# Performance work log

Measured on AMD Instinct MI355X. Metric: run time of the kernel, lower is better.

Reference implementation:

```python
import jax, jax.numpy as jnp
import numpy as np


def setup_inputs() -> dict:
    key = jax.random.key(0)
    ks = jax.random.split(key, 6)
    B, T, D, H = 64, 2048, 128, 256
    stdv = 1.0 / np.sqrt(H)
    return {
        "X": jax.random.normal(ks[0], (B, T, D), dtype=jnp.float32),
        "W": jax.random.normal(ks[1], (D, 4 * H), dtype=jnp.float32) * stdv,
        "U": jax.random.normal(ks[2], (H, 4 * H), dtype=jnp.float32) * stdv,
        "bias": jax.random.normal(ks[3], (4 * H,), dtype=jnp.float32) * stdv,
        "h0": jax.random.normal(ks[4], (B, H), dtype=jnp.float32) * stdv,
        "c0": jax.random.normal(ks[5], (B, H), dtype=jnp.float32) * stdv,
    }


def reference(X, W, U, bias, h0, c0):
    HS = U.shape[0]
    # Hoist input projection into one big GEMM: [B,T,4H]
    xW = jnp.einsum("btd,dg->btg", X, W) + bias

    def step(carry, xw_t):
        h, c = carry
        gates = xw_t + h @ U  # [B,4H]
        i_t = jax.nn.sigmoid(gates[:, :HS])
        f_t = jax.nn.sigmoid(gates[:, HS:2 * HS])
        g_t = jnp.tanh(gates[:, 2 * HS:3 * HS])
        o_t = jax.nn.sigmoid(gates[:, 3 * HS:])
        c_new = f_t * c + i_t * g_t
        h_new = o_t * jnp.tanh(c_new)
        return (h_new, c_new), h_new

    (h_t, c_t), hs = jax.lax.scan(step, (h0, c0), jnp.swapaxes(xW, 0, 1))
    hidden_seq = jnp.swapaxes(hs, 0, 1)  # [B,T,H]
    return (hidden_seq, (h_t, c_t))
```

## Files before the change

### kernel.cpp

```cpp
#include <hip/hip_runtime.h>
#include <hip/hip_bf16.h>

#define BB 64
#define TT 2048
#define DD 128
#define HH 256
#define G4 1024
#define TC 16

typedef _Float16 half2_t __attribute__((ext_vector_type(2)));

#if __has_builtin(__builtin_amdgcn_fdot2)
#define FDOT2(a, b, c) __builtin_amdgcn_fdot2((a), (b), (c), false)
#else
__device__ __forceinline__ float FDOT2(half2_t a, half2_t b, float c) {
    return c + (float)a[0] * (float)b[0] + (float)a[1] * (float)b[1];
}
#endif

__device__ __forceinline__ half2_t u2h(unsigned int u) {
    union { unsigned int u; half2_t h; } x; x.u = u; return x.h;
}
__device__ __forceinline__ unsigned int pkf16(float a, float b) {
    union { _Float16 h[2]; unsigned int u; } x;
    x.h[0] = (_Float16)a; x.h[1] = (_Float16)b; return x.u;
}
__device__ __forceinline__ unsigned short f16b(float a) {
    union { _Float16 h; unsigned short u; } x; x.h = (_Float16)a; return x.u;
}
__device__ __forceinline__ float sigf(float x) {
    return 1.0f / (1.0f + __expf(-x));
}
__device__ __forceinline__ float tanh_fast(float x) {
    return 1.0f - 2.0f / (__expf(2.0f * x) + 1.0f);
}
__device__ __forceinline__ void bar_lgkm() {
    asm volatile("s_waitcnt lgkmcnt(0)\n\ts_barrier" ::: "memory");
}

__global__ void zero_hglob(unsigned long long* hglob) {
    hglob[blockIdx.x * 256 + threadIdx.x] = 0ull;
}

__global__ void __launch_bounds__(128)
pack_slices(const float* __restrict__ src, unsigned short* __restrict__ dst, int K)
{
    const int g = blockIdx.x, kb = blockIdx.y, c = threadIdx.x;
    const int gc = ((c >> 5) << 8) + (g << 5) + (c & 31);
    unsigned int* d32 = (unsigned int*)dst;
    const int dbase = ((g << 7) + c) * K + kb * 64;
    for (int kk = 0; kk < 64; kk += 2) {
        const float a = src[(size_t)(kb * 64 + kk) * G4 + gc];
        const float b = src[(size_t)(kb * 64 + kk + 1) * G4 + gc];
        d32[(dbase + kk) >> 1] = pkf16(a, b);
    }
}

extern "C" __global__ void __launch_bounds__(512, 2)
lstm_fuse(const float* __restrict__ X, const unsigned short* __restrict__ Upack,
          const unsigned short* __restrict__ Wpack, const float* __restrict__ bias,
          const float* __restrict__ h0, const float* __restrict__ c0,
          unsigned long long* __restrict__ hglob, float* __restrict__ out)
{
    __shared__ __align__(16) uint4 Ulds4[128 * 32];
    __shared__ __align__(16) uint4 Wlds4[128 * 16];
    __shared__ float xw[2][TC][128];
    __shared__ __align__(16) unsigned short Xs[2 * TC * DD];
    __shared__ float gvp[2][4][128];
    __shared__ __align__(16) unsigned short hsh[2 * HH];

    const int pair = blockIdx.x & 31;
    const int g = blockIdx.x >> 5;
    const int b0 = pair * 2;
    const int tid = threadIdx.x;
    const int wave = tid >> 6, lane = tid & 63;
    const int c = tid & 127, s = tid >> 7;

    {
        const uint4* Usrc = (const uint4*)(Upack + (size_t)g * 32768);
        #pragma unroll
        for (int i = 0; i < 8; ++i) {
            const int idx = i * 512 + tid;
            const int cc = idx >> 5, gr = idx & 31;
            Ulds4[cc * 32 + (gr ^ (cc & 31))] = Usrc[idx];
        }
        const uint4* Wsrc = (const uint4*)(Wpack + (size_t)g * 16384);
        #pragma unroll
        for (int i = 0; i < 4; ++i) {
            const int idx = i * 512 + tid;
            const int cc = idx >> 4, gr = idx & 15;
            Wlds4[cc * 16 + (gr ^ (cc & 15))] = Wsrc[idx];
        }
    }
    hsh[tid] = f16b(h0[(size_t)(b0 + (tid >> 8)) * HH + (tid & 255)]);
    float c_reg = 0.0f, h_last = 0.0f;
    if (wave == 0) {
        const int p = lane >> 5, j = lane & 31;
        c_reg = c0[(size_t)(b0 + p) * HH + (g << 5) + j];
        h_last = h0[(size_t)(b0 + p) * HH + (g << 5) + j];
    }
    const float bc = bias[((c >> 5) << 8) + (g << 5) + (c & 31)];
    __syncthreads();

    const size_t obase0 = (size_t)b0 * TT * HH + (g << 5);
    const size_t obase1 = (size_t)(b0 + 1) * TT * HH + (g << 5);
    const int slotbase = ((pair << 3) + g) << 1;

    for (int chunk = 0; chunk < TT / TC; ++chunk) {
        const int t0 = chunk * TC;

        #pragma unroll
        for (int r = 0; r < 2; ++r) {
            const float4 xv = ((const float4*)(X + ((size_t)(b0 + r) * TT + t0) * DD))[tid];
            ((uint2*)Xs)[r * 512 + tid] = make_uint2(pkf16(xv.x, xv.y), pkf16(xv.z, xv.w));
        }
        bar_lgkm();

        {
            const int p = s >> 1, th = s & 1;
            float acc[8];
            #pragma unroll
            for (int t = 0; t < 8; ++t) acc[t] = bc;
            #pragma unroll
            for (int k8 = 0; k8 < 16; ++k8) {
                const uint4 w4 = Wlds4[c * 16 + (k8 ^ (c & 15))];
                #pragma unroll
                for (int t = 0; t < 8; ++t) {
                    const uint4 xg = *(const uint4*)((const char*)Xs +
                                     ((p * 16 + th * 8 + t) << 8) + (k8 << 4));
                    acc[t] = FDOT2(u2h(xg.x), u2h(w4.x), acc[t]);
                    acc[t] = FDOT2(u2h(xg.y), u2h(w4.y), acc[t]);
                    acc[t] = FDOT2(u2h(xg.z), u2h(w4.z), acc[t]);
                    acc[t] = FDOT2(u2h(xg.w), u2h(w4.w), acc[t]);
                }
            }
            #pragma unroll
            for (int t = 0; t < 8; ++t) xw[p][th * 8 + t][c] = acc[t];
        }
        bar_lgkm();

        for (int tt2 = 0; tt2 < TC; ++tt2) {
            const int tau = t0 + tt2;

            {
                float a0 = (s == 0) ? xw[0][tt2][c] : 0.0f;
                float a1 = (s == 0) ? xw[1][tt2][c] : 0.0f;
                #pragma unroll
                for (int ii = 0; ii < 8; ++ii) {
                    const uint4 ug = Ulds4[c * 32 + ((s * 8 + ii) ^ (c & 31))];
                    const uint4 hg0 = *(const uint4*)((const char*)hsh + (s << 7) + (ii << 4));
                    const uint4 hg1 = *(const uint4*)((const char*)hsh + 512 + (s << 7) + (ii << 4));
                    a0 = FDOT2(u2h(ug.x), u2h(hg0.x), a0);
                    a1 = FDOT2(u2h(ug.x), u2h(hg1.x), a1);
                    a0 = FDOT2(u2h(ug.y), u2h(hg0.y), a0);
                    a1 = FDOT2(u2h(ug.y), u2h(hg1.y), a1);
                    a0 = FDOT2(u2h(ug.z), u2h(hg0.z), a0);
                    a1 = FDOT2(u2h(ug.z), u2h(hg1.z), a1);
                    a0 = FDOT2(u2h(ug.w), u2h(hg0.w), a0);
                    a1 = FDOT2(u2h(ug.w), u2h(hg1.w), a1);
                }
                gvp[0][s][c] = a0;
                gvp[1][s][c] = a1;
            }
            bar_lgkm();

            const int par = (tau + 1) & 1;
            if (wave == 0) {
                const int p = lane >> 5, j = lane & 31;
                const float* gv = &gvp[p][0][0];
                float gi = 0.f, gf = 0.f, gg = 0.f, go = 0.f;
                #pragma unroll
                for (int q = 0; q < 4; ++q) {
                    gi += gv[q * 128 + j];       gf += gv[q * 128 + 32 + j];
                    gg += gv[q * 128 + 64 + j];  go += gv[q * 128 + 96 + j];
                }
                const float it = sigf(gi), ft = sigf(gf);
                const float gt = tanh_fast(gg), ot = sigf(go);
                c_reg = fmaf(ft, c_reg, it * gt);
                const float hn = ot * tanh_fast(c_reg);
                h_last = hn;
                const unsigned int hu = f16b(hn);
                const unsigned int lo = __shfl((int)hu, j);
                const unsigned int hi = __shfl((int)hu, j + 32);
                if (lane < 32) {
                    const unsigned long long pkt =
                        ((unsigned long long)(unsigned)(tau + 1) << 32) |
                        ((unsigned long long)hi << 16) | (unsigned long long)lo;
                    __hip_atomic_store(&hglob[(size_t)(slotbase + par) * 32 + j],
                                       pkt, __ATOMIC_RELAXED, __HIP_MEMORY_SCOPE_AGENT);
                }
                out[(p ? obase1 : obase0) + (size_t)tau * HH + j] = hn;
                hsh[(p << 8) + (g << 5) + j] = (unsigned short)hu;
            } else if (tau < TT - 1 && lane < 32) {
                const int pg = (g + wave) & 7;
                const unsigned long long* q =
                    &hglob[(size_t)((((pair << 3) + pg) << 1) + par) * 32 + lane];
                __builtin_amdgcn_s_sleep(2);
                unsigned long long v; int spins = 0;
                do {
                    v = __hip_atomic_load(q, __ATOMIC_RELAXED, __HIP_MEMORY_SCOPE_AGENT);
                    if (++spins > (1 << 20)) break;
                } while ((unsigned)(v >> 32) != (unsigned)(tau + 1));
                hsh[(pg << 5) + lane] = (unsigned short)(v & 0xffff);
                hsh[256 + (pg << 5) + lane] = (unsigned short)((v >> 16) & 0xffff);
            }
            bar_lgkm();
        }
    }

    if (wave == 0) {
        const int p = lane >> 5, j = lane & 31;
        const size_t base = (size_t)BB * TT * HH;
        out[base + (size_t)(b0 + p) * HH + (g << 5) + j] = h_last;
        out[base + (size_t)BB * HH + (size_t)(b0 + p) * HH + (g << 5) + j] = c_reg;
    }
}

extern "C" __global__ void __launch_bounds__(512)
lstm_persist(const float* __restrict__ X, const float* __restrict__ W,
             const float* __restrict__ U, const float* __restrict__ bias,
             const float* __restrict__ h0, const float* __restrict__ c0,
             float* __restrict__ out)
{
    __shared__ float xw[TC][G4];
    __shared__ float Xs[TC][DD];
    __shared__ float hsh[HH];
    __shared__ float gv[G4];

    const int b = blockIdx.x;
    const int tid = threadIdx.x;
    const float2* __restrict__ U2 = reinterpret_cast<const float2*>(U);
    const float2* __restrict__ W2 = reinterpret_cast<const float2*>(W);

    float c_reg = 0.0f;
    if (tid < HH) { hsh[tid] = h0[b * HH + tid]; c_reg = c0[b * HH + tid]; }
    const float2 bs = reinterpret_cast<const float2*>(bias)[tid];
    __syncthreads();

    for (int chunk = 0; chunk < TT / TC; ++chunk) {
        const int t0 = chunk * TC;
        {
            const float4* src = reinterpret_cast<const float4*>(X + ((size_t)b * TT + t0) * DD);
            float4* dst = reinterpret_cast<float4*>(&Xs[0][0]);
            for (int i = tid; i < TC * DD / 4; i += 512) dst[i] = src[i];
        }
        __syncthreads();
        float acc0[TC], acc1[TC];
        #pragma unroll
        for (int t = 0; t < TC; ++t) { acc0[t] = bs.x; acc1[t] = bs.y; }
        for (int kk = 0; kk < DD; kk += 4) {
            const float2 w0 = W2[(size_t)(kk + 0) * (G4 / 2) + tid];
            const float2 w1 = W2[(size_t)(kk + 1) * (G4 / 2) + tid];
            const float2 w2 = W2[(size_t)(kk + 2) * (G4 / 2) + tid];
            const float2 w3 = W2[(size_t)(kk + 3) * (G4 / 2) + tid];
            #pragma unroll
            for (int t = 0; t < TC; ++t) {
                const float4 xv = *reinterpret_cast<const float4*>(&Xs[t][kk]);
                acc0[t] = fmaf(xv.x, w0.x, acc0[t]); acc1[t] = fmaf(xv.x, w0.y, acc1[t]);
                acc0[t] = fmaf(xv.y, w1.x, acc0[t]); acc1[t] = fmaf(xv.y, w1.y, acc1[t]);
                acc0[t] = fmaf(xv.z, w2.x, acc0[t]); acc1[t] = fmaf(xv.z, w2.y, acc1[t]);
                acc0[t] = fmaf(xv.w, w3.x, acc0[t]); acc1[t] = fmaf(xv.w, w3.y, acc1[t]);
            }
        }
        #pragma unroll
        for (int t = 0; t < TC; ++t)
            *reinterpret_cast<float2*>(&xw[t][2 * tid]) = make_float2(acc0[t], acc1[t]);
        __syncthreads();

        for (int t = 0; t < TC; ++t) {
            const float2 x2 = *reinterpret_cast<const float2*>(&xw[t][2 * tid]);
            float a0 = x2.x, a1 = x2.y;
            #pragma unroll 4
            for (int k = 0; k < HH; k += 4) {
                const float4 hk = *reinterpret_cast<const float4*>(&hsh[k]);
                const float2 u0 = U2[(size_t)(k + 0) * (G4 / 2) + tid];
                const float2 u1 = U2[(size_t)(k + 1) * (G4 / 2) + tid];
                const float2 u2 = U2[(size_t)(k + 2) * (G4 / 2) + tid];
                const float2 u3 = U2[(size_t)(k + 3) * (G4 / 2) + tid];
                a0 = fmaf(hk.x, u0.x, a0); a1 = fmaf(hk.x, u0.y, a1);
                a0 = fmaf(hk.y, u1.x, a0); a1 = fmaf(hk.y, u1.y, a1);
                a0 = fmaf(hk.z, u2.x, a0); a1 = fmaf(hk.z, u2.y, a1);
                a0 = fmaf(hk.w, u3.x, a0); a1 = fmaf(hk.w, u3.y, a1);
            }
            *reinterpret_cast<float2*>(&gv[2 * tid]) = make_float2(a0, a1);
            __syncthreads();
            if (tid < HH) {
                const float it = sigf(gv[tid]);
                const float ft = sigf(gv[tid + HH]);
                const float gt = tanh_fast(gv[tid + 2 * HH]);
                const float ot = sigf(gv[tid + 3 * HH]);
                c_reg = fmaf(ft, c_reg, it * gt);
                const float hn = ot * tanh_fast(c_reg);
                hsh[tid] = hn;
                out[((size_t)b * TT + (t0 + t)) * HH + tid] = hn;
            }
            __syncthreads();
        }
    }
    if (tid < HH) {
        const size_t base = (size_t)BB * TT * HH;
        out[base + (size_t)b * HH + tid] = hsh[tid];
        out[base + (size_t)BB * HH + (size_t)b * HH + tid] = c_reg;
    }
}

extern "C" void kernel_launch(void* const* d_in, const int* in_sizes, int n_in,
                              void* d_out, int out_size, void* d_ws, size_t ws_size,
                              hipStream_t stream) {
    const float* X    = (const float*)d_in[0];
    const float* W    = (const float*)d_in[1];
    const float* U    = (const float*)d_in[2];
    const float* bias = (const float*)d_in[3];
    const float* h0   = (const float*)d_in[4];
    const float* c0   = (const float*)d_in[5];
    float* out = (float*)d_out;
    (void)in_sizes; (void)n_in; (void)out_size;

    const size_t upk = 512 * 1024;
    const size_t wpk = 256 * 1024;
    const size_t mbx = 128 * 1024;

    if (ws_size >= upk + wpk + mbx) {
        unsigned short* Upack = (unsigned short*)d_ws;
        unsigned short* Wpack = (unsigned short*)((char*)d_ws + upk);
        unsigned long long* hglob = (unsigned long long*)((char*)d_ws + upk + wpk);
        zero_hglob<<<dim3(64), dim3(256), 0, stream>>>(hglob);
        pack_slices<<<dim3(8, 4), dim3(128), 0, stream>>>(U, Upack, 256);
        pack_slices<<<dim3(8, 2), dim3(128), 0, stream>>>(W, Wpack, 128);
        lstm_fuse<<<dim3(256), dim3(512), 0, stream>>>(
            X, Upack, Wpack, bias, h0, c0, hglob, out);
        return;
    }

    lstm_persist<<<dim3(BB), dim3(512), 0, stream>>>(X, W, U, bias, h0, c0, out);
}
```

Baseline: 3.568 ms.

## Widen LSTM recurrent blocks to 1024 threads with eight-way K split

Doubles the threads per block from 512 to 1024. The recurrent h@U dot product is now split over 8 K-slices instead of 4, and the input projection over 4 timestep groups per batch row. The xW term moves from the first partial sum into the gate reduction in wave 0. Peer-h polling now uses two redundant trains of 7 waves, one with a longer sleep, to cut the latency of seeing a neighbour's update. This shortens the per-step serial dot-product chain, at the cost of more partial-sum reduction, more LDS traffic, and one block per CU under the new launch bounds.

```diff
diff --git a/kernel.cpp b/kernel.cpp
--- a/kernel.cpp
+++ b/kernel.cpp
@@ -56,8 +56,8 @@
     }
 }
 
-extern "C" __global__ void __launch_bounds__(512, 2)
-lstm_fuse(const float* __restrict__ X, const unsigned short* __restrict__ Upack,
+extern "C" __global__ void __launch_bounds__(1024, 1)
+lstm_wide(const float* __restrict__ X, const unsigned short* __restrict__ Upack,
           const unsigned short* __restrict__ Wpack, const float* __restrict__ bias,
           const float* __restrict__ h0, const float* __restrict__ c0,
           unsigned long long* __restrict__ hglob, float* __restrict__ out)
@@ -66,7 +66,7 @@
     __shared__ __align__(16) uint4 Wlds4[128 * 16];
     __shared__ float xw[2][TC][128];
     __shared__ __align__(16) unsigned short Xs[2 * TC * DD];
-    __shared__ float gvp[2][4][128];
+    __shared__ float gvp[2][8][128];
     __shared__ __align__(16) unsigned short hsh[2 * HH];
 
     const int pair = blockIdx.x & 31;
@@ -79,20 +79,21 @@
     {
         const uint4* Usrc = (const uint4*)(Upack + (size_t)g * 32768);
         #pragma unroll
-        for (int i = 0; i < 8; ++i) {
-            const int idx = i * 512 + tid;
+        for (int i = 0; i < 4; ++i) {
+            const int idx = i * 1024 + tid;
             const int cc = idx >> 5, gr = idx & 31;
             Ulds4[cc * 32 + (gr ^ (cc & 31))] = Usrc[idx];
         }
         const uint4* Wsrc = (const uint4*)(Wpack + (size_t)g * 16384);
         #pragma unroll
-        for (int i = 0; i < 4; ++i) {
-            const int idx = i * 512 + tid;
+        for (int i = 0; i < 2; ++i) {
+            const int idx = i * 1024 + tid;
             const int cc = idx >> 4, gr = idx & 15;
             Wlds4[cc * 16 + (gr ^ (cc & 15))] = Wsrc[idx];
         }
     }
-    hsh[tid] = f16b(h0[(size_t)(b0 + (tid >> 8)) * HH + (tid & 255)]);
+    if (tid < 512)
+        hsh[tid] = f16b(h0[(size_t)(b0 + (tid >> 8)) * HH + (tid & 255)]);
     float c_reg = 0.0f, h_last = 0.0f;
     if (wave == 0) {
         const int p = lane >> 5, j = lane & 31;
@@ -111,23 +112,23 @@
 
         #pragma unroll
         for (int r = 0; r < 2; ++r) {
-            const float4 xv = ((const float4*)(X + ((size_t)(b0 + r) * TT + t0) * DD))[tid];
-            ((uint2*)Xs)[r * 512 + tid] = make_uint2(pkf16(xv.x, xv.y), pkf16(xv.z, xv.w));
+            const float2 v = ((const float2*)(X + ((size_t)(b0 + r) * TT + t0) * DD))[tid];
+            ((unsigned int*)Xs)[r * 1024 + tid] = pkf16(v.x, v.y);
         }
         bar_lgkm();
 
         {
-            const int p = s >> 1, th = s & 1;
-            float acc[8];
+            const int p = s >> 2, tq = s & 3;
+            float acc[4];
             #pragma unroll
-            for (int t = 0; t < 8; ++t) acc[t] = bc;
+            for (int t = 0; t < 4; ++t) acc[t] = bc;
             #pragma unroll
             for (int k8 = 0; k8 < 16; ++k8) {
                 const uint4 w4 = Wlds4[c * 16 + (k8 ^ (c & 15))];
                 #pragma unroll
-                for (int t = 0; t < 8; ++t) {
+                for (int t = 0; t < 4; ++t) {
                     const uint4 xg = *(const uint4*)((const char*)Xs +
-                                     ((p * 16 + th * 8 + t) << 8) + (k8 << 4));
+                                     ((p * 16 + tq * 4 + t) << 8) + (k8 << 4));
                     acc[t] = FDOT2(u2h(xg.x), u2h(w4.x), acc[t]);
                     acc[t] = FDOT2(u2h(xg.y), u2h(w4.y), acc[t]);
                     acc[t] = FDOT2(u2h(xg.z), u2h(w4.z), acc[t]);
@@ -135,7 +136,7 @@
                 }
             }
             #pragma unroll
-            for (int t = 0; t < 8; ++t) xw[p][th * 8 + t][c] = acc[t];
+            for (int t = 0; t < 4; ++t) xw[p][tq * 4 + t][c] = acc[t];
         }
         bar_lgkm();
 
@@ -143,13 +144,13 @@
             const int tau = t0 + tt2;
 
             {
-                float a0 = (s == 0) ? xw[0][tt2][c] : 0.0f;
-                float a1 = (s == 0) ? xw[1][tt2][c] : 0.0f;
+                float a0 = 0.0f, a1 = 0.0f;
                 #pragma unroll
-                for (int ii = 0; ii < 8; ++ii) {
-                    const uint4 ug = Ulds4[c * 32 + ((s * 8 + ii) ^ (c & 31))];
-                    const uint4 hg0 = *(const uint4*)((const char*)hsh + (s << 7) + (ii << 4));
-                    const uint4 hg1 = *(const uint4*)((const char*)hsh + 512 + (s << 7) + (ii << 4));
+                for (int ii = 0; ii < 4; ++ii) {
+                    const int k8 = s * 4 + ii;
+                    const uint4 ug = Ulds4[c * 32 + (k8 ^ (c & 31))];
+                    const uint4 hg0 = *(const uint4*)((const char*)hsh + (k8 << 4));
+                    const uint4 hg1 = *(const uint4*)((const char*)hsh + 512 + (k8 << 4));
                     a0 = FDOT2(u2h(ug.x), u2h(hg0.x), a0);
                     a1 = FDOT2(u2h(ug.x), u2h(hg1.x), a1);
                     a0 = FDOT2(u2h(ug.y), u2h(hg0.y), a0);
@@ -167,12 +168,14 @@
             const int par = (tau + 1) & 1;
             if (wave == 0) {
                 const int p = lane >> 5, j = lane & 31;
-                const float* gv = &gvp[p][0][0];
-                float gi = 0.f, gf = 0.f, gg = 0.f, go = 0.f;
+                float gi = xw[p][tt2][j];
+                float gf = xw[p][tt2][32 + j];
+                float gg = xw[p][tt2][64 + j];
+                float go = xw[p][tt2][96 + j];
                 #pragma unroll
-                for (int q = 0; q < 4; ++q) {
-                    gi += gv[q * 128 + j];       gf += gv[q * 128 + 32 + j];
-                    gg += gv[q * 128 + 64 + j];  go += gv[q * 128 + 96 + j];
+                for (int q = 0; q < 8; ++q) {
+                    gi += gvp[p][q][j];       gf += gvp[p][q][32 + j];
+                    gg += gvp[p][q][64 + j];  go += gvp[p][q][96 + j];
                 }
                 const float it = sigf(gi), ft = sigf(gf);
                 const float gt = tanh_fast(gg), ot = sigf(go);
@@ -191,11 +194,13 @@
                 }
                 out[(p ? obase1 : obase0) + (size_t)tau * HH + j] = hn;
                 hsh[(p << 8) + (g << 5) + j] = (unsigned short)hu;
-            } else if (tau < TT - 1 && lane < 32) {
-                const int pg = (g + wave) & 7;
+            } else if (wave <= 14 && tau < TT - 1 && lane < 32) {
+                const int pw = ((wave - 1) % 7) + 1;
+                const int train = (wave - 1) / 7;
+                const int pg = (g + pw) & 7;
                 const unsigned long long* q =
                     &hglob[(size_t)((((pair << 3) + pg) << 1) + par) * 32 + lane];
-                __builtin_amdgcn_s_sleep(2);
+                if (train) __builtin_amdgcn_s_sleep(6);
                 unsigned long long v; int spins = 0;
                 do {
                     v = __hip_atomic_load(q, __ATOMIC_RELAXED, __HIP_MEMORY_SCOPE_AGENT);
@@ -327,7 +332,7 @@
         zero_hglob<<<dim3(64), dim3(256), 0, stream>>>(hglob);
         pack_slices<<<dim3(8, 4), dim3(128), 0, stream>>>(U, Upack, 256);
         pack_slices<<<dim3(8, 2), dim3(128), 0, stream>>>(W, Wpack, 128);
-        lstm_fuse<<<dim3(256), dim3(512), 0, stream>>>(
+        lstm_wide<<<dim3(256), dim3(1024), 0, stream>>>(
             X, Upack, Wpack, bias, h0, c0, hglob, out);
         return;
     }
```

New measurement: 4.074 ms. 1.14x slower.

## Distribute recurrent matvec per source wave to cut per-step barriers

Applied to the files above, without the earlier changes.

Each wave now computes the partial h·U contribution for the 32-column h slice it owns: wave 0 handles its own freshly computed slice, and the other waves handle the neighbour slices they poll from global memory. Partial sums are written into double-buffered gvp[nxt] and reduced in the next step together with xw. This removes one block barrier per timestep and overlaps the matvec with the cross-block exchange. The cost is a larger reduction (8 partials) and more LDS traffic per step, and launch bounds drop to one block per CU.

```diff
diff --git a/kernel.cpp b/kernel.cpp
--- a/kernel.cpp
+++ b/kernel.cpp
@@ -36,6 +36,9 @@
 }
 __device__ __forceinline__ void bar_lgkm() {
     asm volatile("s_waitcnt lgkmcnt(0)\n\ts_barrier" ::: "memory");
+}
+__device__ __forceinline__ void wait_lgkm() {
+    asm volatile("s_waitcnt lgkmcnt(0)" ::: "memory");
 }
 
 __global__ void zero_hglob(unsigned long long* hglob) {
@@ -56,8 +59,8 @@
     }
 }
 
-extern "C" __global__ void __launch_bounds__(512, 2)
-lstm_fuse(const float* __restrict__ X, const unsigned short* __restrict__ Upack,
+extern "C" __global__ void __launch_bounds__(512, 1)
+lstm_dist(const float* __restrict__ X, const unsigned short* __restrict__ Upack,
           const unsigned short* __restrict__ Wpack, const float* __restrict__ bias,
           const float* __restrict__ h0, const float* __restrict__ c0,
           unsigned long long* __restrict__ hglob, float* __restrict__ out)
@@ -66,8 +69,9 @@
     __shared__ __align__(16) uint4 Wlds4[128 * 16];
     __shared__ float xw[2][TC][128];
     __shared__ __align__(16) unsigned short Xs[2 * TC * DD];
-    __shared__ float gvp[2][4][128];
-    __shared__ __align__(16) unsigned short hsh[2 * HH];
+    __shared__ float gvp[2][2][8][128];
+    __shared__ __align__(16) unsigned short hst0[8][32];
+    __shared__ __align__(16) unsigned short hst1[8][32];
 
     const int pair = blockIdx.x & 31;
     const int g = blockIdx.x >> 5;
@@ -92,7 +96,6 @@
             Wlds4[cc * 16 + (gr ^ (cc & 15))] = Wsrc[idx];
         }
     }
-    hsh[tid] = f16b(h0[(size_t)(b0 + (tid >> 8)) * HH + (tid & 255)]);
     float c_reg = 0.0f, h_last = 0.0f;
     if (wave == 0) {
         const int p = lane >> 5, j = lane & 31;
@@ -100,6 +103,35 @@
         h_last = h0[(size_t)(b0 + p) * HH + (g << 5) + j];
     }
     const float bc = bias[((c >> 5) << 8) + (g << 5) + (c & 31)];
+
+    {
+        const int pg = (g + wave) & 7;
+        if (lane < 32) {
+            hst0[wave][lane] = f16b(h0[(size_t)b0 * HH + (pg << 5) + lane]);
+            hst1[wave][lane] = f16b(h0[(size_t)(b0 + 1) * HH + (pg << 5) + lane]);
+        }
+        wait_lgkm();
+        const int c0l = lane, c1l = lane + 64;
+        float a00 = 0.f, a01 = 0.f, a10 = 0.f, a11 = 0.f;
+        #pragma unroll
+        for (int ks = 0; ks < 4; ++ks) {
+            const int k8 = (pg << 2) + ks;
+            const uint4 u0 = Ulds4[c0l * 32 + (k8 ^ (c0l & 31))];
+            const uint4 u1 = Ulds4[c1l * 32 + (k8 ^ (c1l & 31))];
+            const uint4 hv0 = *(const uint4*)((const char*)&hst0[wave][0] + (ks << 4));
+            const uint4 hv1 = *(const uint4*)((const char*)&hst1[wave][0] + (ks << 4));
+            a00 = FDOT2(u2h(u0.x), u2h(hv0.x), a00); a01 = FDOT2(u2h(u0.x), u2h(hv1.x), a01);
+            a10 = FDOT2(u2h(u1.x), u2h(hv0.x), a10); a11 = FDOT2(u2h(u1.x), u2h(hv1.x), a11);
+            a00 = FDOT2(u2h(u0.y), u2h(hv0.y), a00); a01 = FDOT2(u2h(u0.y), u2h(hv1.y), a01);
+            a10 = FDOT2(u2h(u1.y), u2h(hv0.y), a10); a11 = FDOT2(u2h(u1.y), u2h(hv1.y), a11);
+            a00 = FDOT2(u2h(u0.z), u2h(hv0.z), a00); a01 = FDOT2(u2h(u0.z), u2h(hv1.z), a01);
+            a10 = FDOT2(u2h(u1.z), u2h(hv0.z), a10); a11 = FDOT2(u2h(u1.z), u2h(hv1.z), a11);
+            a00 = FDOT2(u2h(u0.w), u2h(hv0.w), a00); a01 = FDOT2(u2h(u0.w), u2h(hv1.w), a01);
+            a10 = FDOT2(u2h(u1.w), u2h(hv0.w), a10); a11 = FDOT2(u2h(u1.w), u2h(hv1.w), a11);
+        }
+        gvp[0][0][wave][c0l] = a00;  gvp[0][1][wave][c0l] = a01;
+        gvp[0][0][wave][c1l] = a10;  gvp[0][1][wave][c1l] = a11;
+    }
     __syncthreads();
 
     const size_t obase0 = (size_t)b0 * TT * HH + (g << 5);
@@ -140,69 +172,94 @@
         bar_lgkm();
 
         for (int tt2 = 0; tt2 < TC; ++tt2) {
-            const int tau = t0 + tt2;
-
-            {
-                float a0 = (s == 0) ? xw[0][tt2][c] : 0.0f;
-                float a1 = (s == 0) ? xw[1][tt2][c] : 0.0f;
-                #pragma unroll
-                for (int ii = 0; ii < 8; ++ii) {
-                    const uint4 ug = Ulds4[c * 32 + ((s * 8 + ii) ^ (c & 31))];
-                    const uint4 hg0 = *(const uint4*)((const char*)hsh + (s << 7) + (ii << 4));
-                    const uint4 hg1 = *(const uint4*)((const char*)hsh + 512 + (s << 7) + (ii << 4));
-                    a0 = FDOT2(u2h(ug.x), u2h(hg0.x), a0);
-                    a1 = FDOT2(u2h(ug.x), u2h(hg1.x), a1);
-                    a0 = FDOT2(u2h(ug.y), u2h(hg0.y), a0);
-                    a1 = FDOT2(u2h(ug.y), u2h(hg1.y), a1);
-                    a0 = FDOT2(u2h(ug.z), u2h(hg0.z), a0);
-                    a1 = FDOT2(u2h(ug.z), u2h(hg1.z), a1);
-                    a0 = FDOT2(u2h(ug.w), u2h(hg0.w), a0);
-                    a1 = FDOT2(u2h(ug.w), u2h(hg1.w), a1);
-                }
-                gvp[0][s][c] = a0;
-                gvp[1][s][c] = a1;
-            }
-            bar_lgkm();
-
-            const int par = (tau + 1) & 1;
+            const int it = t0 + tt2;
+            const int cur = it & 1, nxt = cur ^ 1;
+            const int par = (it + 1) & 1;
+
             if (wave == 0) {
                 const int p = lane >> 5, j = lane & 31;
-                const float* gv = &gvp[p][0][0];
-                float gi = 0.f, gf = 0.f, gg = 0.f, go = 0.f;
+                const float* xr = &xw[p][tt2][0];
+                float gi = xr[j], gf = xr[32 + j], gg = xr[64 + j], go = xr[96 + j];
                 #pragma unroll
-                for (int q = 0; q < 4; ++q) {
-                    gi += gv[q * 128 + j];       gf += gv[q * 128 + 32 + j];
-                    gg += gv[q * 128 + 64 + j];  go += gv[q * 128 + 96 + j];
-                }
-                const float it = sigf(gi), ft = sigf(gf);
+                for (int q = 0; q < 8; ++q) {
+                    const float* gq = &gvp[cur][p][q][0];
+                    gi += gq[j]; gf += gq[32 + j]; gg += gq[64 + j]; go += gq[96 + j];
+                }
+                const float it_g = sigf(gi), ft = sigf(gf);
                 const float gt = tanh_fast(gg), ot = sigf(go);
-                c_reg = fmaf(ft, c_reg, it * gt);
+                c_reg = fmaf(ft, c_reg, it_g * gt);
                 const float hn = ot * tanh_fast(c_reg);
                 h_last = hn;
                 const unsigned int hu = f16b(hn);
                 const unsigned int lo = __shfl((int)hu, j);
                 const unsigned int hi = __shfl((int)hu, j + 32);
-                if (lane < 32) {
+                if (it < TT - 1 && lane < 32) {
                     const unsigned long long pkt =
-                        ((unsigned long long)(unsigned)(tau + 1) << 32) |
+                        ((unsigned long long)(unsigned)(it + 1) << 32) |
                         ((unsigned long long)hi << 16) | (unsigned long long)lo;
                     __hip_atomic_store(&hglob[(size_t)(slotbase + par) * 32 + j],
                                        pkt, __ATOMIC_RELAXED, __HIP_MEMORY_SCOPE_AGENT);
-                }
-                out[(p ? obase1 : obase0) + (size_t)tau * HH + j] = hn;
-                hsh[(p << 8) + (g << 5) + j] = (unsigned short)hu;
-            } else if (tau < TT - 1 && lane < 32) {
+                    hst0[0][j] = (unsigned short)lo;
+                    hst1[0][j] = (unsigned short)hi;
+                }
+                out[(p ? obase1 : obase0) + (size_t)it * HH + j] = hn;
+                if (it < TT - 1) {
+                    wait_lgkm();
+                    const int c0l = lane, c1l = lane + 64;
+                    float a00 = 0.f, a01 = 0.f, a10 = 0.f, a11 = 0.f;
+                    #pragma unroll
+                    for (int ks = 0; ks < 4; ++ks) {
+                        const int k8 = (g << 2) + ks;
+                        const uint4 u0 = Ulds4[c0l * 32 + (k8 ^ (c0l & 31))];
+                        const uint4 u1 = Ulds4[c1l * 32 + (k8 ^ (c1l & 31))];
+                        const uint4 hv0 = *(const uint4*)((const char*)&hst0[0][0] + (ks << 4));
+                        const uint4 hv1 = *(const uint4*)((const char*)&hst1[0][0] + (ks << 4));
+                        a00 = FDOT2(u2h(u0.x), u2h(hv0.x), a00); a01 = FDOT2(u2h(u0.x), u2h(hv1.x), a01);
+                        a10 = FDOT2(u2h(u1.x), u2h(hv0.x), a10); a11 = FDOT2(u2h(u1.x), u2h(hv1.x), a11);
+                        a00 = FDOT2(u2h(u0.y), u2h(hv0.y), a00); a01 = FDOT2(u2h(u0.y), u2h(hv1.y), a01);
+                        a10 = FDOT2(u2h(u1.y), u2h(hv0.y), a10); a11 = FDOT2(u2h(u1.y), u2h(hv1.y), a11);
+                        a00 = FDOT2(u2h(u0.z), u2h(hv0.z), a00); a01 = FDOT2(u2h(u0.z), u2h(hv1.z), a01);
+                        a10 = FDOT2(u2h(u1.z), u2h(hv0.z), a10); a11 = FDOT2(u2h(u1.z), u2h(hv1.z), a11);
+                        a00 = FDOT2(u2h(u0.w), u2h(hv0.w), a00); a01 = FDOT2(u2h(u0.w), u2h(hv1.w), a01);
+                        a10 = FDOT2(u2h(u1.w), u2h(hv0.w), a10); a11 = FDOT2(u2h(u1.w), u2h(hv1.w), a11);
+                    }
+                    gvp[nxt][0][0][c0l] = a00;  gvp[nxt][1][0][c0l] = a01;
+                    gvp[nxt][0][0][c1l] = a10;  gvp[nxt][1][0][c1l] = a11;
+                }
+            } else if (it < TT - 1) {
                 const int pg = (g + wave) & 7;
-                const unsigned long long* q =
-                    &hglob[(size_t)((((pair << 3) + pg) << 1) + par) * 32 + lane];
-                __builtin_amdgcn_s_sleep(2);
-                unsigned long long v; int spins = 0;
-                do {
-                    v = __hip_atomic_load(q, __ATOMIC_RELAXED, __HIP_MEMORY_SCOPE_AGENT);
-                    if (++spins > (1 << 20)) break;
-                } while ((unsigned)(v >> 32) != (unsigned)(tau + 1));
-                hsh[(pg << 5) + lane] = (unsigned short)(v & 0xffff);
-                hsh[256 + (pg << 5) + lane] = (unsigned short)((v >> 16) & 0xffff);
+                if (lane < 32) {
+                    const unsigned long long* q =
+                        &hglob[(size_t)((((pair << 3) + pg) << 1) + par) * 32 + lane];
+                    unsigned long long v; int spins = 0;
+                    do {
+                        v = __hip_atomic_load(q, __ATOMIC_RELAXED, __HIP_MEMORY_SCOPE_AGENT);
+                        if (++spins > (1 << 20)) break;
+                    } while ((unsigned)(v >> 32) != (unsigned)(it + 1));
+                    hst0[wave][lane] = (unsigned short)(v & 0xffff);
+                    hst1[wave][lane] = (unsigned short)((v >> 16) & 0xffff);
+                }
+                wait_lgkm();
+                const int c0l = lane, c1l = lane + 64;
+                float a00 = 0.f, a01 = 0.f, a10 = 0.f, a11 = 0.f;
+                #pragma unroll
+                for (int ks = 0; ks < 4; ++ks) {
+                    const int k8 = (pg << 2) + ks;
+                    const uint4 u0 = Ulds4[c0l * 32 + (k8 ^ (c0l & 31))];
+                    const uint4 u1 = Ulds4[c1l * 32 + (k8 ^ (c1l & 31))];
+                    const uint4 hv0 = *(const uint4*)((const char*)&hst0[wave][0] + (ks << 4));
+                    const uint4 hv1 = *(const uint4*)((const char*)&hst1[wave][0] + (ks << 4));
+                    a00 = FDOT2(u2h(u0.x), u2h(hv0.x), a00); a01 = FDOT2(u2h(u0.x), u2h(hv1.x), a01);
+                    a10 = FDOT2(u2h(u1.x), u2h(hv0.x), a10); a11 = FDOT2(u2h(u1.x), u2h(hv1.x), a11);
+                    a00 = FDOT2(u2h(u0.y), u2h(hv0.y), a00); a01 = FDOT2(u2h(u0.y), u2h(hv1.y), a01);
+                    a10 = FDOT2(u2h(u1.y), u2h(hv0.y), a10); a11 = FDOT2(u2h(u1.y), u2h(hv1.y), a11);
+                    a00 = FDOT2(u2h(u0.z), u2h(hv0.z), a00); a01 = FDOT2(u2h(u0.z), u2h(hv1.z), a01);
+                    a10 = FDOT2(u2h(u1.z), u2h(hv0.z), a10); a11 = FDOT2(u2h(u1.z), u2h(hv1.z), a11);
+                    a00 = FDOT2(u2h(u0.w), u2h(hv0.w), a00); a01 = FDOT2(u2h(u0.w), u2h(hv1.w), a01);
+                    a10 = FDOT2(u2h(u1.w), u2h(hv0.w), a10); a11 = FDOT2(u2h(u1.w), u2h(hv1.w), a11);
+                }
+                gvp[nxt][0][wave][c0l] = a00;  gvp[nxt][1][wave][c0l] = a01;
+                gvp[nxt][0][wave][c1l] = a10;  gvp[nxt][1][wave][c1l] = a11;
             }
             bar_lgkm();
         }
@@ -327,7 +384,7 @@
         zero_hglob<<<dim3(64), dim3(256), 0, stream>>>(hglob);
         pack_slices<<<dim3(8, 4), dim3(128), 0, stream>>>(U, Upack, 256);
         pack_slices<<<dim3(8, 2), dim3(128), 0, stream>>>(W, Wpack, 128);
-        lstm_fuse<<<dim3(256), dim3(512), 0, stream>>>(
+        lstm_dist<<<dim3(256), dim3(512), 0, stream>>>(
             X, Upack, Wpack, bias, h0, c0, hglob, out);
         return;
     }
```

New measurement: 3.624 ms. About the same (+1.6%).

## Stagger two batch rows per block to overlap recurrence exchange with compute

Applied to the files above, without the earlier changes.

Each block now processes its two batch rows in alternating half-steps. Row 0's matvec runs while row 1's hidden-state slices from peer blocks are still arriving, and the reverse, so the cross-block spin-wait latency is hidden behind the other row's compute. Mailbox slots are split per row, each carrying an fp32 h value, which doubles the mailbox workspace and the zeroing grid. It also raises the priority of the activation wave and removes the sleep before polling. The cost is twice as many barriers per time step and narrower per-step work.

```diff
diff --git a/kernel.cpp b/kernel.cpp
--- a/kernel.cpp
+++ b/kernel.cpp
@@ -57,7 +57,7 @@
 }
 
 extern "C" __global__ void __launch_bounds__(512, 2)
-lstm_fuse(const float* __restrict__ X, const unsigned short* __restrict__ Upack,
+lstm_pipe(const float* __restrict__ X, const unsigned short* __restrict__ Upack,
           const unsigned short* __restrict__ Wpack, const float* __restrict__ bias,
           const float* __restrict__ h0, const float* __restrict__ c0,
           unsigned long long* __restrict__ hglob, float* __restrict__ out)
@@ -66,7 +66,7 @@
     __shared__ __align__(16) uint4 Wlds4[128 * 16];
     __shared__ float xw[2][TC][128];
     __shared__ __align__(16) unsigned short Xs[2 * TC * DD];
-    __shared__ float gvp[2][4][128];
+    __shared__ float gvp[4][128];
     __shared__ __align__(16) unsigned short hsh[2 * HH];
 
     const int pair = blockIdx.x & 31;
@@ -93,11 +93,12 @@
         }
     }
     hsh[tid] = f16b(h0[(size_t)(b0 + (tid >> 8)) * HH + (tid & 255)]);
-    float c_reg = 0.0f, h_last = 0.0f;
-    if (wave == 0) {
-        const int p = lane >> 5, j = lane & 31;
-        c_reg = c0[(size_t)(b0 + p) * HH + (g << 5) + j];
-        h_last = h0[(size_t)(b0 + p) * HH + (g << 5) + j];
+    float c_reg0 = 0.0f, c_reg1 = 0.0f, h_last0 = 0.0f, h_last1 = 0.0f;
+    if (wave == 0 && lane < 32) {
+        c_reg0 = c0[(size_t)b0 * HH + (g << 5) + lane];
+        c_reg1 = c0[(size_t)(b0 + 1) * HH + (g << 5) + lane];
+        h_last0 = h0[(size_t)b0 * HH + (g << 5) + lane];
+        h_last1 = h0[(size_t)(b0 + 1) * HH + (g << 5) + lane];
     }
     const float bc = bias[((c >> 5) << 8) + (g << 5) + (c & 31)];
     __syncthreads();
@@ -143,76 +144,117 @@
             const int tau = t0 + tt2;
 
             {
-                float a0 = (s == 0) ? xw[0][tt2][c] : 0.0f;
-                float a1 = (s == 0) ? xw[1][tt2][c] : 0.0f;
+                float a = (s == 0) ? xw[0][tt2][c] : 0.0f;
                 #pragma unroll
                 for (int ii = 0; ii < 8; ++ii) {
                     const uint4 ug = Ulds4[c * 32 + ((s * 8 + ii) ^ (c & 31))];
-                    const uint4 hg0 = *(const uint4*)((const char*)hsh + (s << 7) + (ii << 4));
-                    const uint4 hg1 = *(const uint4*)((const char*)hsh + 512 + (s << 7) + (ii << 4));
-                    a0 = FDOT2(u2h(ug.x), u2h(hg0.x), a0);
-                    a1 = FDOT2(u2h(ug.x), u2h(hg1.x), a1);
-                    a0 = FDOT2(u2h(ug.y), u2h(hg0.y), a0);
-                    a1 = FDOT2(u2h(ug.y), u2h(hg1.y), a1);
-                    a0 = FDOT2(u2h(ug.z), u2h(hg0.z), a0);
-                    a1 = FDOT2(u2h(ug.z), u2h(hg1.z), a1);
-                    a0 = FDOT2(u2h(ug.w), u2h(hg0.w), a0);
-                    a1 = FDOT2(u2h(ug.w), u2h(hg1.w), a1);
-                }
-                gvp[0][s][c] = a0;
-                gvp[1][s][c] = a1;
+                    const uint4 hg = *(const uint4*)((const char*)hsh + (s << 7) + (ii << 4));
+                    a = FDOT2(u2h(ug.x), u2h(hg.x), a);
+                    a = FDOT2(u2h(ug.y), u2h(hg.y), a);
+                    a = FDOT2(u2h(ug.z), u2h(hg.z), a);
+                    a = FDOT2(u2h(ug.w), u2h(hg.w), a);
+                }
+                gvp[s][c] = a;
             }
             bar_lgkm();
 
-            const int par = (tau + 1) & 1;
             if (wave == 0) {
-                const int p = lane >> 5, j = lane & 31;
-                const float* gv = &gvp[p][0][0];
-                float gi = 0.f, gf = 0.f, gg = 0.f, go = 0.f;
-                #pragma unroll
-                for (int q = 0; q < 4; ++q) {
-                    gi += gv[q * 128 + j];       gf += gv[q * 128 + 32 + j];
-                    gg += gv[q * 128 + 64 + j];  go += gv[q * 128 + 96 + j];
-                }
-                const float it = sigf(gi), ft = sigf(gf);
-                const float gt = tanh_fast(gg), ot = sigf(go);
-                c_reg = fmaf(ft, c_reg, it * gt);
-                const float hn = ot * tanh_fast(c_reg);
-                h_last = hn;
-                const unsigned int hu = f16b(hn);
-                const unsigned int lo = __shfl((int)hu, j);
-                const unsigned int hi = __shfl((int)hu, j + 32);
+                __builtin_amdgcn_s_setprio(1);
                 if (lane < 32) {
+                    const int j = lane;
+                    float gi = 0.f, gf = 0.f, gg = 0.f, go = 0.f;
+                    #pragma unroll
+                    for (int q = 0; q < 4; ++q) {
+                        gi += gvp[q][j];       gf += gvp[q][32 + j];
+                        gg += gvp[q][64 + j];  go += gvp[q][96 + j];
+                    }
+                    const float it = sigf(gi), ft = sigf(gf);
+                    const float gt = tanh_fast(gg), ot = sigf(go);
+                    c_reg0 = fmaf(ft, c_reg0, it * gt);
+                    const float hn = ot * tanh_fast(c_reg0);
+                    h_last0 = hn;
                     const unsigned long long pkt =
                         ((unsigned long long)(unsigned)(tau + 1) << 32) |
-                        ((unsigned long long)hi << 16) | (unsigned long long)lo;
-                    __hip_atomic_store(&hglob[(size_t)(slotbase + par) * 32 + j],
+                        (unsigned long long)__float_as_uint(hn);
+                    __hip_atomic_store(&hglob[(size_t)(slotbase + ((tau + 1) & 1)) * 64 + j],
                                        pkt, __ATOMIC_RELAXED, __HIP_MEMORY_SCOPE_AGENT);
-                }
-                out[(p ? obase1 : obase0) + (size_t)tau * HH + j] = hn;
-                hsh[(p << 8) + (g << 5) + j] = (unsigned short)hu;
+                    out[obase0 + (size_t)tau * HH + j] = hn;
+                    hsh[(g << 5) + j] = f16b(hn);
+                }
+                __builtin_amdgcn_s_setprio(0);
+            } else if (tau >= 1 && lane < 32) {
+                const int pg = (g + wave) & 7;
+                const unsigned long long* q =
+                    &hglob[(size_t)((((pair << 3) + pg) << 1) + (tau & 1)) * 64 + 32 + lane];
+                unsigned long long v; int spins = 0;
+                do {
+                    v = __hip_atomic_load(q, __ATOMIC_RELAXED, __HIP_MEMORY_SCOPE_AGENT);
+                    if (++spins > (1 << 20)) break;
+                } while ((unsigned)(v >> 32) != (unsigned)tau);
+                hsh[256 + (pg << 5) + lane] = f16b(__uint_as_float((unsigned)v));
+            }
+            bar_lgkm();
+
+            {
+                float a = (s == 0) ? xw[1][tt2][c] : 0.0f;
+                #pragma unroll
+                for (int ii = 0; ii < 8; ++ii) {
+                    const uint4 ug = Ulds4[c * 32 + ((s * 8 + ii) ^ (c & 31))];
+                    const uint4 hg = *(const uint4*)((const char*)hsh + 512 + (s << 7) + (ii << 4));
+                    a = FDOT2(u2h(ug.x), u2h(hg.x), a);
+                    a = FDOT2(u2h(ug.y), u2h(hg.y), a);
+                    a = FDOT2(u2h(ug.z), u2h(hg.z), a);
+                    a = FDOT2(u2h(ug.w), u2h(hg.w), a);
+                }
+                gvp[s][c] = a;
+            }
+            bar_lgkm();
+
+            if (wave == 0) {
+                __builtin_amdgcn_s_setprio(1);
+                if (lane < 32) {
+                    const int j = lane;
+                    float gi = 0.f, gf = 0.f, gg = 0.f, go = 0.f;
+                    #pragma unroll
+                    for (int q = 0; q < 4; ++q) {
+                        gi += gvp[q][j];       gf += gvp[q][32 + j];
+                        gg += gvp[q][64 + j];  go += gvp[q][96 + j];
+                    }
+                    const float it = sigf(gi), ft = sigf(gf);
+                    const float gt = tanh_fast(gg), ot = sigf(go);
+                    c_reg1 = fmaf(ft, c_reg1, it * gt);
+                    const float hn = ot * tanh_fast(c_reg1);
+                    h_last1 = hn;
+                    const unsigned long long pkt =
+                        ((unsigned long long)(unsigned)(tau + 1) << 32) |
+                        (unsigned long long)__float_as_uint(hn);
+                    __hip_atomic_store(&hglob[(size_t)(slotbase + ((tau + 1) & 1)) * 64 + 32 + j],
+                                       pkt, __ATOMIC_RELAXED, __HIP_MEMORY_SCOPE_AGENT);
+                    out[obase1 + (size_t)tau * HH + j] = hn;
+                    hsh[256 + (g << 5) + j] = f16b(hn);
+                }
+                __builtin_amdgcn_s_setprio(0);
             } else if (tau < TT - 1 && lane < 32) {
                 const int pg = (g + wave) & 7;
                 const unsigned long long* q =
-                    &hglob[(size_t)((((pair << 3) + pg) << 1) + par) * 32 + lane];
-                __builtin_amdgcn_s_sleep(2);
+                    &hglob[(size_t)((((pair << 3) + pg) << 1) + ((tau + 1) & 1)) * 64 + lane];
                 unsigned long long v; int spins = 0;
                 do {
                     v = __hip_atomic_load(q, __ATOMIC_RELAXED, __HIP_MEMORY_SCOPE_AGENT);
                     if (++spins > (1 << 20)) break;
                 } while ((unsigned)(v >> 32) != (unsigned)(tau + 1));
-                hsh[(pg << 5) + lane] = (unsigned short)(v & 0xffff);
-                hsh[256 + (pg << 5) + lane] = (unsigned short)((v >> 16) & 0xffff);
+                hsh[(pg << 5) + lane] = f16b(__uint_as_float((unsigned)v));
             }
             bar_lgkm();
         }
     }
 
-    if (wave == 0) {
-        const int p = lane >> 5, j = lane & 31;
+    if (wave == 0 && lane < 32) {
         const size_t base = (size_t)BB * TT * HH;
-        out[base + (size_t)(b0 + p) * HH + (g << 5) + j] = h_last;
-        out[base + (size_t)BB * HH + (size_t)(b0 + p) * HH + (g << 5) + j] = c_reg;
+        out[base + (size_t)b0 * HH + (g << 5) + lane] = h_last0;
+        out[base + (size_t)(b0 + 1) * HH + (g << 5) + lane] = h_last1;
+        out[base + (size_t)BB * HH + (size_t)b0 * HH + (g << 5) + lane] = c_reg0;
+        out[base + (size_t)BB * HH + (size_t)(b0 + 1) * HH + (g << 5) + lane] = c_reg1;
     }
 }
 
@@ -318,16 +360,16 @@
 
     const size_t upk = 512 * 1024;
     const size_t wpk = 256 * 1024;
-    const size_t mbx = 128 * 1024;
+    const size_t mbx = 256 * 1024;
 
     if (ws_size >= upk + wpk + mbx) {
         unsigned short* Upack = (unsigned short*)d_ws;
         unsigned short* Wpack = (unsigned short*)((char*)d_ws + upk);
         unsigned long long* hglob = (unsigned long long*)((char*)d_ws + upk + wpk);
-        zero_hglob<<<dim3(64), dim3(256), 0, stream>>>(hglob);
+        zero_hglob<<<dim3(128), dim3(256), 0, stream>>>(hglob);
         pack_slices<<<dim3(8, 4), dim3(128), 0, stream>>>(U, Upack, 256);
         pack_slices<<<dim3(8, 2), dim3(128), 0, stream>>>(W, Wpack, 128);
-        lstm_fuse<<<dim3(256), dim3(512), 0, stream>>>(
+        lstm_pipe<<<dim3(256), dim3(512), 0, stream>>>(
             X, Upack, Wpack, bias, h0, c0, hglob, out);
         return;
     }
```

Measured after the change: 3.521 ms. About the same (-1.3%).
